# Performance work log

Measured on AMD Instinct MI355X. Metric: run time of the kernel, lower is better.

## Reference

```python
import jax, jax.numpy as jnp
import numpy as np

EPS = 1e-5
NUM_HEADS = 12

def layer_norm(x, g, b):
    mu = jnp.mean(x, axis=-1, keepdims=True)
    var = jnp.var(x, axis=-1, keepdims=True)
    return (x - mu) * jax.lax.rsqrt(var + EPS) * g + b

def setup_inputs() -> dict:
    key = jax.random.key(0)
    ks = jax.random.split(key, 8)
    B, N, Dv, Ds, F = 8, 1024, 768, 512, 768
    def w(k, shape, fan_in):
        return jax.random.normal(k, shape, jnp.float32) * (fan_in ** -0.5)
    return dict(
        visual_features=jax.random.normal(ks[0], (B, N, Dv), jnp.float32),
        semantic_features=jax.random.normal(ks[1], (B, Ds), jnp.float32),
        Wq=w(ks[2], (F, Ds), Ds),
        Wk=w(ks[3], (F, Dv), Dv),
        Wv=w(ks[4], (F, Dv), Dv),
        Wo=w(ks[5], (Dv, F), F),
        bo=jnp.zeros((Dv,), jnp.float32),
        Wg=w(ks[6], (Dv, Dv + Ds), Dv + Ds),
        bg=jnp.zeros((Dv,), jnp.float32),
        gv=jnp.ones((Dv,), jnp.float32),
        bv=jnp.zeros((Dv,), jnp.float32),
        gs=jnp.ones((Ds,), jnp.float32),
        bs=jnp.zeros((Ds,), jnp.float32),
    )

def reference(visual_features, semantic_features, Wq, Wk, Wv, Wo, bo, Wg, bg, gv, bv, gs, bs):
    B, N, Dv = visual_features.shape
    F = Wq.shape[0]
    H = NUM_HEADS
    dh = F // H
    scale = dh ** -0.5
    vis_n = layer_norm(visual_features, gv, bv)           # (B,N,Dv)
    sem_n = layer_norm(semantic_features, gs, bs)         # (B,Ds) — LN over last dim; broadcast-invariant
    # Query is identical for every patch row -> exact single-query collapse of the N x N attention
    q = (sem_n @ Wq.T).reshape(B, H, dh)                  # (B,H,dh)
    k = (vis_n @ Wk.T).reshape(B, N, H, dh).transpose(0, 2, 1, 3)  # (B,H,N,dh)
    v = (vis_n @ Wv.T).reshape(B, N, H, dh).transpose(0, 2, 1, 3)  # (B,H,N,dh)
    scores = jnp.einsum('bhd,bhnd->bhn', q, k) * scale
    attn = jax.nn.softmax(scores, axis=-1)
    ctx = jnp.einsum('bhn,bhnd->bhd', attn, v).reshape(B, F)
    attended = ctx @ Wo.T + bo                            # (B,Dv), same for all N rows (dropout in eval = identity)
    sem_b = jnp.broadcast_to(semantic_features[:, None, :], (B, N, semantic_features.shape[-1]))
    gate_in = jnp.concatenate([visual_features, sem_b], axis=-1)   # (B,N,Dv+Ds)
    gate = jax.nn.sigmoid(gate_in @ Wg.T + bg)            # (B,N,Dv)
    return visual_features + gate * attended[:, None, :]
```

## Files before the change

### kernel.cpp

```cpp
#include <hip/hip_runtime.h>
#include <hip/hip_bf16.h>
#include <math.h>


typedef __attribute__((ext_vector_type(8))) short bf16x8;
typedef __attribute__((ext_vector_type(4))) float f32x4;

#define LN_EPS 1e-5f

__device__ __forceinline__ float bf2f(__hip_bfloat16 h){ return __bfloat162float(h); }

union bfpk8 { uint4 u; __hip_bfloat16 h[8]; };
union bfpk4 { uint2 u; __hip_bfloat16 h[4]; };

__device__ __align__(16) __hip_bfloat16 c_x[8*1024*768];
__device__ __align__(16) __hip_bfloat16 c_sem[8*512];
__device__ __align__(16) __hip_bfloat16 c_Wq[768*512];
__device__ __align__(16) __hip_bfloat16 c_Wk[768*768];
__device__ __align__(16) __hip_bfloat16 c_Wv[768*768];
__device__ __align__(16) __hip_bfloat16 c_Wo[768*768];
__device__ __align__(16) __hip_bfloat16 c_bo[768];
__device__ __align__(16) __hip_bfloat16 c_Wg[768*1280];
__device__ __align__(16) __hip_bfloat16 c_bg[768];
__device__ __align__(16) __hip_bfloat16 c_gv[768];
__device__ __align__(16) __hip_bfloat16 c_bv[768];
__device__ __align__(16) __hip_bfloat16 c_gs[512];
__device__ __align__(16) __hip_bfloat16 c_bs[512];

__device__ __align__(16) __hip_bfloat16 g_gqb[8*16*768];
__device__ __align__(16) float g_A[8*12*768];
__device__ __align__(16) float g_sgq[96];
__device__ __align__(16) float g_bq[96];
__device__ __align__(16) float g_mu[8192];
__device__ __align__(16) float g_rstd[8192];
__device__ __align__(16) float g_w[8*12*1024];
__device__ __align__(16) float g_C[96];
__device__ __align__(16) float g_ctx[8*768];
__device__ __align__(16) float g_att[8*768];
__device__ __align__(16) float g_gsem[8*768];

__device__ __forceinline__ int detect_bf16(const void* gv_raw){
    return ((const unsigned int*)gv_raw)[0] == 0x3F803F80u;
}

__device__ __forceinline__ void conv8(const void* __restrict__ src,
                                      __hip_bfloat16* __restrict__ dst,
                                      int g, int isb){
    if(isb){
        ((uint4*)dst)[g] = ((const uint4*)src)[g];
    } else {
        const float* s = (const float*)src + (size_t)g*8;
        bfpk8 o;
        #pragma unroll
        for(int e=0;e<8;e++) o.h[e] = __float2bfloat16(s[e]);
        ((uint4*)dst)[g] = o.u;
    }
}

#define ING_BLKS 1925
__global__ void k_ingest(const void* s1, const void* s2, const void* s3,
                         const void* s4, const void* s5, const void* s6, const void* s7,
                         const void* s8, const void* s9, const void* s10, const void* s11,
                         const void* s12){
    int i = blockIdx.x*256 + threadIdx.x;
    int isb = detect_bf16(s9);
    if     (i <    512) conv8(s1, c_sem, i,         isb);
    else if(i <  49664) conv8(s2, c_Wq,  i-   512,  isb);
    else if(i < 123392) conv8(s3, c_Wk,  i- 49664,  isb);
    else if(i < 197120) conv8(s4, c_Wv,  i-123392,  isb);
    else if(i < 270848) conv8(s5, c_Wo,  i-197120,  isb);
    else if(i < 270944) conv8(s6, c_bo,  i-270848,  isb);
    else if(i < 393824) conv8(s7, c_Wg,  i-270944,  isb);
    else if(i < 393920) conv8(s8, c_bg,  i-393824,  isb);
    else if(i < 394016) conv8(s9, c_gv,  i-393920,  isb);
    else if(i < 394112) conv8(s10,c_bv,  i-394016,  isb);
    else if(i < 394176) conv8(s11,c_gs,  i-394112,  isb);
    else if(i < 394240) conv8(s12,c_bs,  i-394176,  isb);
    else if(i < 467968) g_A[i-394240]   = 0.f;
    else if(i < 468064) g_sgq[i-467968] = 0.f;
    else if(i < 468160) g_bq[i-468064]  = 0.f;
    else if(i < 474304) g_ctx[i-468160] = 0.f;
    else if(i < 480448) g_att[i-474304] = 0.f;
    else if(i < 492736){
        uint4 z; z.x=0; z.y=0; z.z=0; z.w=0;
        ((uint4*)g_gqb)[i-480448] = z;
    }
}

__global__ void k_qhead(){
    __shared__ float s_semn[8*512];
    __shared__ float s_q2[8][64];
    __shared__ float s_sgq[8], s_bq[8];
    const int t = threadIdx.x, h = blockIdx.y;
    {
        int b = t>>5, l = t&31;
        bfpk8 p0, p1;
        p0.u = *(const uint4*)(c_sem + b*512 + l*16);
        p1.u = *(const uint4*)(c_sem + b*512 + l*16 + 8);
        float v[16], s = 0.f, s2 = 0.f;
        #pragma unroll
        for(int e=0;e<8;e++){ v[e]   = bf2f(p0.h[e]); s += v[e];   s2 += v[e]*v[e]; }
        #pragma unroll
        for(int e=0;e<8;e++){ v[8+e] = bf2f(p1.h[e]); s += v[8+e]; s2 += v[8+e]*v[8+e]; }
        #pragma unroll
        for(int o=16;o>0;o>>=1){ s += __shfl_xor(s,o); s2 += __shfl_xor(s2,o); }
        float mu = s*(1.f/512.f);
        float rstd = rsqrtf(s2*(1.f/512.f) - mu*mu + LN_EPS);
        bfpk8 g0, g1, b0, b1;
        g0.u = *(const uint4*)(c_gs + l*16);   g1.u = *(const uint4*)(c_gs + l*16 + 8);
        b0.u = *(const uint4*)(c_bs + l*16);   b1.u = *(const uint4*)(c_bs + l*16 + 8);
        #pragma unroll
        for(int e=0;e<8;e++){
            s_semn[b*512 + l*16 + e]     = (v[e]-mu)*rstd*bf2f(g0.h[e]) + bf2f(b0.h[e]);
            s_semn[b*512 + l*16 + 8 + e] = (v[8+e]-mu)*rstd*bf2f(g1.h[e]) + bf2f(b1.h[e]);
        }
    }
    if(t < 8){ s_sgq[t] = 0.f; s_bq[t] = 0.f; }
    __syncthreads();
    {
        int fi = t & 63, bp = t >> 6;
        int f = h*64 + fi;
        const __hip_bfloat16* wr = c_Wq + (size_t)f*512;
        float a0 = 0.f, a1 = 0.f;
        for(int i0=0;i0<512;i0+=8){
            bfpk8 pk; pk.u = *(const uint4*)(wr + i0);
            #pragma unroll
            for(int c=0;c<8;c++){
                float wv = bf2f(pk.h[c]);
                a0 += wv*s_semn[bp*512 + i0 + c];
                a1 += wv*s_semn[(bp+4)*512 + i0 + c];
            }
        }
        s_q2[bp][fi] = a0; s_q2[bp+4][fi] = a1;
    }
    __syncthreads();
    int dv = blockIdx.x*256 + t;
    float acc[8] = {0,0,0,0,0,0,0,0};
    for(int j=0;j<64;j++){
        float wk = bf2f(c_Wk[(size_t)(h*64+j)*768 + dv]);
        #pragma unroll
        for(int b=0;b<8;b++) acc[b] += s_q2[b][j]*wk;
    }
    float gvv = bf2f(c_gv[dv]), bvv = bf2f(c_bv[dv]);
    #pragma unroll
    for(int b=0;b<8;b++){
        float g = acc[b]*gvv;
        g_gqb[((size_t)b*16+h)*768 + dv] = __float2bfloat16(g);
        float sg = g, sb = bvv*acc[b];
        #pragma unroll
        for(int o=32;o>0;o>>=1){ sg += __shfl_xor(sg,o); sb += __shfl_xor(sb,o); }
        if((t&63)==0){ atomicAdd(&s_sgq[b], sg); atomicAdd(&s_bq[b], sb); }
    }
    __syncthreads();
    if(t < 8){ atomicAdd(&g_sgq[t*12+h], s_sgq[t]); atomicAdd(&g_bq[t*12+h], s_bq[t]); }
}

__global__ __launch_bounds__(256)
void k_gsem(){
    __shared__ float s_sem[8*512];
    __shared__ __hip_bfloat16 s_wg[16*520];
    __shared__ float s_part[128];
    const int t = threadIdx.x;
    const int col0 = blockIdx.x*16;
    for(int i=t;i<512;i+=256){
        bfpk8 p; p.u = *(const uint4*)(c_sem + i*8);
        #pragma unroll
        for(int e=0;e<8;e++) s_sem[i*8+e] = bf2f(p.h[e]);
    }
    for(int i=t;i<16*64;i+=256){
        int rl = i>>6, c = i&63;
        *(uint4*)(s_wg + rl*520 + c*8) =
            *(const uint4*)(c_Wg + (size_t)(col0+rl)*1280 + 768 + c*8);
    }
    __syncthreads();
    const int cl = t&15, bh = t>>4, bb = bh&7, half = bh>>3;
    const __hip_bfloat16* wr = s_wg + cl*520 + half*256;
    const float* sr = s_sem + bb*512 + half*256;
    float a = 0.f;
    for(int k=0;k<256;k+=8){
        bfpk8 p; p.u = *(const uint4*)(wr + k);
        #pragma unroll
        for(int e=0;e<8;e++) a += bf2f(p.h[e])*sr[k+e];
    }
    if(half) s_part[t&127] = a;
    __syncthreads();
    if(!half) g_gsem[bb*768 + col0 + cl] = a + s_part[t&127];
}

__global__ __launch_bounds__(256)
void k_scores(const void* __restrict__ xraw, const void* __restrict__ gvraw){
    __shared__ float s_acc[256*4];
    __shared__ float s_s[4][16], s_s2[4][16];
    __shared__ float s_mu[16], s_rstd[16];
    const int b = blockIdx.y;
    const int t = threadIdx.x, lane = t & 63, w = t >> 6;
    const int isb = detect_bf16(gvraw);
    const int fr = lane & 15, quad = lane >> 4;
    const int n_tile = blockIdx.x*16;
    const size_t row = (size_t)b*1024 + n_tile + fr;
    const __hip_bfloat16* Bp = g_gqb + (size_t)b*16*768 + (size_t)fr*768;
    const int k0 = w*192;

    f32x4 acc = {};
    float s = 0.f, s2 = 0.f;
    if(isb){
        const __hip_bfloat16* xr = (const __hip_bfloat16*)xraw + row*768;
        for(int kb=k0; kb<k0+192; kb+=32){
            bfpk8 pk; pk.u = *(const uint4*)(xr + kb + quad*8);
            *(uint4*)(c_x + row*768 + kb + quad*8) = pk.u;
            #pragma unroll
            for(int e=0;e<8;e++){ float f = bf2f(pk.h[e]); s += f; s2 += f*f; }
            bf16x8 bfrag = *(const bf16x8*)(Bp + kb + quad*8);
            acc = __builtin_amdgcn_mfma_f32_16x16x32_bf16(*(const bf16x8*)&pk, bfrag, acc, 0,0,0);
        }
    } else {
        const float* xr = (const float*)xraw + row*768;
        for(int kb=k0; kb<k0+192; kb+=32){
            f32x4 x0 = *(const f32x4*)(xr + kb + quad*8);
            f32x4 x1 = *(const f32x4*)(xr + kb + quad*8 + 4);
            bfpk8 pk;
            #pragma unroll
            for(int e=0;e<4;e++){ pk.h[e]   = __float2bfloat16(x0[e]); s += x0[e]; s2 += x0[e]*x0[e]; }
            #pragma unroll
            for(int e=0;e<4;e++){ pk.h[4+e] = __float2bfloat16(x1[e]); s += x1[e]; s2 += x1[e]*x1[e]; }
            *(uint4*)(c_x + row*768 + kb + quad*8) = pk.u;
            bf16x8 bfrag = *(const bf16x8*)(Bp + kb + quad*8);
            acc = __builtin_amdgcn_mfma_f32_16x16x32_bf16(*(const bf16x8*)&pk, bfrag, acc, 0,0,0);
        }
    }
    s  += __shfl_xor(s, 16);  s  += __shfl_xor(s, 32);
    s2 += __shfl_xor(s2, 16); s2 += __shfl_xor(s2, 32);
    *(f32x4*)&s_acc[t*4] = acc;
    if(quad == 0){ s_s[w][fr] = s; s_s2[w][fr] = s2; }
    __syncthreads();
    if(w == 0){
        #pragma unroll
        for(int ww=1;ww<4;ww++){
            f32x4 o = *(const f32x4*)&s_acc[(ww*64+lane)*4];
            acc[0]+=o[0]; acc[1]+=o[1]; acc[2]+=o[2]; acc[3]+=o[3];
        }
        if(quad == 0){
            float st  = s_s[0][fr]+s_s[1][fr]+s_s[2][fr]+s_s[3][fr];
            float st2 = s_s2[0][fr]+s_s2[1][fr]+s_s2[2][fr]+s_s2[3][fr];
            float mu = st*(1.f/768.f);
            float rstd = rsqrtf(st2*(1.f/768.f) - mu*mu + LN_EPS);
            g_mu[b*1024 + n_tile + fr] = mu;
            g_rstd[b*1024 + n_tile + fr] = rstd;
            s_mu[fr] = mu; s_rstd[fr] = rstd;
        }
    }
    __syncthreads();
    if(w == 0 && fr < 12){
        float sgqh = g_sgq[b*12+fr];
        float bqh  = g_bq [b*12+fr];
        #pragma unroll
        for(int r=0;r<4;r++){
            int rr = quad*4 + r;
            float val = 0.125f*( s_rstd[rr]*(acc[r] - s_mu[rr]*sgqh) + bqh );
            g_w[((size_t)b*12+fr)*1024 + n_tile + rr] = val;
        }
    }
}

__global__ void k_softmax(){
    int bh = blockIdx.x, b = bh/12, t = threadIdx.x;
    float* sc = g_w + (size_t)bh*1024;
    f32x4 v = *(f32x4*)(sc + t*4);
    float m = fmaxf(fmaxf(v[0],v[1]), fmaxf(v[2],v[3]));
    __shared__ float redm[4], reds[4], redc[4];
    #pragma unroll
    for(int o=32;o>0;o>>=1) m = fmaxf(m, __shfl_xor(m,o));
    if((t&63)==0) redm[t>>6] = m;
    __syncthreads();
    m = fmaxf(fmaxf(redm[0],redm[1]), fmaxf(redm[2],redm[3]));
    float e0=expf(v[0]-m), e1=expf(v[1]-m), e2=expf(v[2]-m), e3=expf(v[3]-m);
    float s = e0+e1+e2+e3;
    #pragma unroll
    for(int o=32;o>0;o>>=1) s += __shfl_xor(s,o);
    if((t&63)==0) reds[t>>6] = s;
    __syncthreads();
    s = reds[0]+reds[1]+reds[2]+reds[3];
    float inv = 1.f/s;
    f32x4 rv = *(f32x4*)(g_rstd + b*1024 + t*4);
    f32x4 mv = *(f32x4*)(g_mu   + b*1024 + t*4);
    f32x4 o4;
    o4[0]=e0*inv*rv[0]; o4[1]=e1*inv*rv[1]; o4[2]=e2*inv*rv[2]; o4[3]=e3*inv*rv[3];
    *(f32x4*)(sc + t*4) = o4;
    float cp = o4[0]*mv[0] + o4[1]*mv[1] + o4[2]*mv[2] + o4[3]*mv[3];
    #pragma unroll
    for(int o=32;o>0;o>>=1) cp += __shfl_xor(cp,o);
    if((t&63)==0) redc[t>>6] = cp;
    __syncthreads();
    if(t==0) g_C[bh] = redc[0]+redc[1]+redc[2]+redc[3];
}

__global__ void k_accA(){
    __shared__ float s_w[12*128];
    int t = threadIdx.x, b = blockIdx.z, n0 = blockIdx.y*128;
    for(int i=t;i<12*128;i+=256){
        int h = i>>7, n = i&127;
        s_w[i] = g_w[((size_t)b*12+h)*1024 + n0 + n];
    }
    __syncthreads();
    int dv = blockIdx.x*256 + t;
    float acc[12] = {0,0,0,0,0,0,0,0,0,0,0,0};
    for(int n=0;n<128;n++){
        float xv = bf2f(c_x[(size_t)(b*1024+n0+n)*768 + dv]);
        #pragma unroll
        for(int h=0;h<12;h++) acc[h] += s_w[h*128+n]*xv;
    }
    #pragma unroll
    for(int h=0;h<12;h++) atomicAdd(&g_A[((size_t)b*12+h)*768 + dv], acc[h]);
}

__global__ void k_ctx(){
    __shared__ float s_wvis[8*68];
    int h = blockIdx.x, ch = blockIdx.y, t = threadIdx.x;
    int base = ch*64;
    {
        int b = t>>6, dvl = t&63;
        int dv = base + dvl;
        s_wvis[b*68+dvl] = bf2f(c_gv[dv])*(g_A[((size_t)b*12+h)*768+dv] - g_C[b*12+h]) + bf2f(c_bv[dv]);
    }
    __syncthreads();
    int f = h*64 + (t>>3), b = t&7;
    const __hip_bfloat16* wr = c_Wv + (size_t)f*768 + base;
    float acc = 0.f;
    #pragma unroll
    for(int d0=0;d0<64;d0+=8){
        bfpk8 pk; pk.u = *(const uint4*)(wr + d0);
        #pragma unroll
        for(int c=0;c<8;c++) acc += s_wvis[b*68 + d0 + c]*bf2f(pk.h[c]);
    }
    atomicAdd(&g_ctx[b*768+f], acc);
}

__global__ void k_att(){
    __shared__ float s_ctx[8*68];
    int ch = blockIdx.y, t = threadIdx.x;
    int base = ch*64;
    {
        int b = t>>6, fl = t&63;
        s_ctx[b*68+fl] = g_ctx[b*768 + base + fl];
    }
    __syncthreads();
    int dv2 = blockIdx.x*64 + (t>>3), b = t&7;
    const __hip_bfloat16* wr = c_Wo + (size_t)dv2*768 + base;
    float acc = (ch==0) ? bf2f(c_bo[dv2]) : 0.f;
    #pragma unroll
    for(int f0=0;f0<64;f0+=8){
        bfpk8 pk; pk.u = *(const uint4*)(wr + f0);
        #pragma unroll
        for(int c=0;c<8;c++) acc += s_ctx[b*68 + f0 + c]*bf2f(pk.h[c]);
    }
    atomicAdd(&g_att[b*768+dv2], acc);
}

__device__ __forceinline__ void stage_gate(int buf, int kb, int m0, int n0,
                                           __hip_bfloat16* As, __hip_bfloat16* Bs,
                                           int wave, int lane){
    const int rl = lane >> 2;
    const int kc = ((lane & 3) ^ ((rl >> 1) & 3))*8;
    #pragma unroll
    for(int s=0;s<2;s++){
        int c = wave + 4*s;
        int row = c*16 + rl;
        const __hip_bfloat16* gp = c_x + (size_t)(m0+row)*768 + kb + kc;
        __builtin_amdgcn_global_load_lds(
            (const __attribute__((address_space(1))) void*)gp,
            (__attribute__((address_space(3))) void*)(As + buf*4096 + c*512),
            16, 0, 0);
    }
    {
        int c = wave;
        int row = c*16 + rl;
        const __hip_bfloat16* gp = c_Wg + (size_t)(n0+row)*1280 + kb + kc;
        __builtin_amdgcn_global_load_lds(
            (const __attribute__((address_space(1))) void*)gp,
            (__attribute__((address_space(3))) void*)(Bs + buf*2048 + c*512),
            16, 0, 0);
    }
}

__global__ __launch_bounds__(256)
void k_gate(void* __restrict__ outv, const void* __restrict__ gv_raw){
    __shared__ __align__(16) __hip_bfloat16 As[4*128*32];
    __shared__ __align__(16) __hip_bfloat16 Bs[4*64*32];
    const int isb = detect_bf16(gv_raw);
    const int t = threadIdx.x;
    const int lin  = blockIdx.y*12 + blockIdx.x;
    const int wgid = (lin & 7)*96 + (lin >> 3);
    const int n0 = (wgid % 12)*64;
    const int m0 = (wgid / 12)*128;
    const int b_blk = m0 >> 10;
    const int lane = t & 63, wave = t >> 6;
    const int wm = (wave>>1)*64, wn = (wave&1)*32;
    const int fr = lane & 15, quad = lane >> 4;
    const int sq = (quad ^ ((fr >> 1) & 3))*8;

    f32x4 acc[4][2] = {};

    stage_gate(0,  0, m0, n0, As, Bs, wave, lane);
    stage_gate(1, 32, m0, n0, As, Bs, wave, lane);
    stage_gate(2, 64, m0, n0, As, Bs, wave, lane);
    for(int it=0; it<24; ++it){
        if(it < 22)       asm volatile("s_waitcnt vmcnt(6)" ::: "memory");
        else if(it == 22) asm volatile("s_waitcnt vmcnt(3)" ::: "memory");
        else              asm volatile("s_waitcnt vmcnt(0)" ::: "memory");
        asm volatile("s_waitcnt lgkmcnt(0)" ::: "memory");
        asm volatile("s_barrier" ::: "memory");
        const __hip_bfloat16* Ab = As + (it&3)*4096;
        const __hip_bfloat16* Bb = Bs + (it&3)*2048;
        bf16x8 af[4], bfr[2];
        #pragma unroll
        for(int i=0;i<4;i++) af[i]  = *(const bf16x8*)(Ab + (wm + i*16 + fr)*32 + sq);
        #pragma unroll
        for(int j=0;j<2;j++) bfr[j] = *(const bf16x8*)(Bb + (wn + j*16 + fr)*32 + sq);
        #pragma unroll
        for(int i=0;i<4;i++)
            #pragma unroll
            for(int j=0;j<2;j++)
                acc[i][j] = __builtin_amdgcn_mfma_f32_16x16x32_bf16(af[i], bfr[j], acc[i][j], 0,0,0);
        if(it < 21)
            stage_gate((it+3)&3, (it+3)*32, m0, n0, As, Bs, wave, lane);
    }

    #pragma unroll
    for(int j=0;j<2;j++){
        int col = n0 + wn + j*16 + fr;
        float attv = g_att[b_blk*768 + col];
        float bgv  = bf2f(c_bg[col]) + g_gsem[b_blk*768 + col];
        #pragma unroll
        for(int i=0;i<4;i++){
            int mbase = m0 + wm + i*16 + quad*4;
            #pragma unroll
            for(int r=0;r<4;r++){
                int m = mbase + r;
                float g = acc[i][j][r] + bgv;
                g = fminf(fmaxf(g, -60.f), 60.f);
                float gate = 1.f/(1.f + expf(-g));
                float xv = bf2f(c_x[(size_t)m*768 + col]);
                float val = xv + gate*attv;
                size_t idx = (size_t)m*768 + col;
                if(isb) ((__hip_bfloat16*)outv)[idx] = __float2bfloat16(val);
                else    ((float*)outv)[idx] = val;
            }
        }
    }
}

extern "C" void kernel_launch(void* const* d_in, const int* in_sizes, int n_in,
                              void* d_out, int out_size, void* d_ws, size_t ws_size,
                              hipStream_t stream){
    (void)in_sizes; (void)n_in; (void)out_size; (void)d_ws; (void)ws_size;

    k_ingest<<<dim3(ING_BLKS), dim3(256), 0, stream>>>(d_in[1], d_in[2], d_in[3],
                                                       d_in[4], d_in[5], d_in[6], d_in[7],
                                                       d_in[8], d_in[9], d_in[10], d_in[11],
                                                       d_in[12]);
    k_qhead<<<dim3(3,12), dim3(256), 0, stream>>>();
    k_gsem<<<dim3(48), dim3(256), 0, stream>>>();
    k_scores<<<dim3(64,8), dim3(256), 0, stream>>>(d_in[0], d_in[9]);
    k_softmax<<<dim3(96), dim3(256), 0, stream>>>();
    k_accA<<<dim3(3,8,8), dim3(256), 0, stream>>>();
    k_ctx<<<dim3(12,12), dim3(512), 0, stream>>>();
    k_att<<<dim3(12,12), dim3(512), 0, stream>>>();
    k_gate<<<dim3(12,64), dim3(256), 0, stream>>>(d_out, d_in[9]);
}
```

Before: 205.0 us.

## Retile q-head projection, drop split-K atomics in ctx/att, prioritize gate MFMAs

k_qhead now runs on a 12x12 grid. Each block stages a 64x64 tile of Wk in LDS and computes two batches per thread instead of eight. The old shared-memory atomic reduction becomes direct global atomics. k_ctx and k_att drop the 12-way split-K with atomicAdd: one block per head (or per output chunk) runs the full 768-long reduction and writes its result directly, which means only 12 blocks with longer serial loops. The gate GEMM wraps its MFMA block in s_setprio to favour the math waves over the loads.

```diff
diff --git a/kernel.cpp b/kernel.cpp
--- a/kernel.cpp
+++ b/kernel.cpp
@@ -87,11 +87,13 @@
     }
 }
 
-__global__ void k_qhead(){
+__global__ __launch_bounds__(256)
+void k_qhead(){
     __shared__ float s_semn[8*512];
     __shared__ float s_q2[8][64];
-    __shared__ float s_sgq[8], s_bq[8];
+    __shared__ __hip_bfloat16 s_wk[64][64];
     const int t = threadIdx.x, h = blockIdx.y;
+    const int c0 = blockIdx.x*64;
     {
         int b = t>>5, l = t&31;
         bfpk8 p0, p1;
@@ -115,7 +117,10 @@
             s_semn[b*512 + l*16 + 8 + e] = (v[8+e]-mu)*rstd*bf2f(g1.h[e]) + bf2f(b1.h[e]);
         }
     }
-    if(t < 8){ s_sgq[t] = 0.f; s_bq[t] = 0.f; }
+    for(int i=t;i<512;i+=256){
+        int j = i>>3, sl = i&7;
+        *(uint4*)(&s_wk[j][sl*8]) = *(const uint4*)(c_Wk + (size_t)(h*64+j)*768 + c0 + sl*8);
+    }
     __syncthreads();
     {
         int fi = t & 63, bp = t >> 6;
@@ -134,25 +139,32 @@
         s_q2[bp][fi] = a0; s_q2[bp+4][fi] = a1;
     }
     __syncthreads();
-    int dv = blockIdx.x*256 + t;
-    float acc[8] = {0,0,0,0,0,0,0,0};
+    const int dvl = t & 63, w = t >> 6;
+    const int dv = c0 + dvl;
+    float a0 = 0.f, a1 = 0.f;
+    #pragma unroll 8
     for(int j=0;j<64;j++){
-        float wk = bf2f(c_Wk[(size_t)(h*64+j)*768 + dv]);
-        #pragma unroll
-        for(int b=0;b<8;b++) acc[b] += s_q2[b][j]*wk;
+        float wk = bf2f(s_wk[j][dvl]);
+        a0 += s_q2[w][j]*wk;
+        a1 += s_q2[w+4][j]*wk;
     }
     float gvv = bf2f(c_gv[dv]), bvv = bf2f(c_bv[dv]);
-    #pragma unroll
-    for(int b=0;b<8;b++){
-        float g = acc[b]*gvv;
-        g_gqb[((size_t)b*16+h)*768 + dv] = __float2bfloat16(g);
-        float sg = g, sb = bvv*acc[b];
+    {
+        float g = a0*gvv;
+        g_gqb[((size_t)w*16+h)*768 + dv] = __float2bfloat16(g);
+        float sg = g, sb = bvv*a0;
         #pragma unroll
         for(int o=32;o>0;o>>=1){ sg += __shfl_xor(sg,o); sb += __shfl_xor(sb,o); }
-        if((t&63)==0){ atomicAdd(&s_sgq[b], sg); atomicAdd(&s_bq[b], sb); }
-    }
-    __syncthreads();
-    if(t < 8){ atomicAdd(&g_sgq[t*12+h], s_sgq[t]); atomicAdd(&g_bq[t*12+h], s_bq[t]); }
+        if(dvl==0){ atomicAdd(&g_sgq[w*12+h], sg); atomicAdd(&g_bq[w*12+h], sb); }
+    }
+    {
+        float g = a1*gvv;
+        g_gqb[((size_t)(w+4)*16+h)*768 + dv] = __float2bfloat16(g);
+        float sg = g, sb = bvv*a1;
+        #pragma unroll
+        for(int o=32;o>0;o>>=1){ sg += __shfl_xor(sg,o); sb += __shfl_xor(sb,o); }
+        if(dvl==0){ atomicAdd(&g_sgq[(w+4)*12+h], sg); atomicAdd(&g_bq[(w+4)*12+h], sb); }
+    }
 }
 
 __global__ __launch_bounds__(256)
@@ -314,46 +326,41 @@
 }
 
 __global__ void k_ctx(){
-    __shared__ float s_wvis[8*68];
-    int h = blockIdx.x, ch = blockIdx.y, t = threadIdx.x;
-    int base = ch*64;
-    {
-        int b = t>>6, dvl = t&63;
-        int dv = base + dvl;
-        s_wvis[b*68+dvl] = bf2f(c_gv[dv])*(g_A[((size_t)b*12+h)*768+dv] - g_C[b*12+h]) + bf2f(c_bv[dv]);
-    }
-    __syncthreads();
-    int f = h*64 + (t>>3), b = t&7;
-    const __hip_bfloat16* wr = c_Wv + (size_t)f*768 + base;
+    __shared__ float s_wvis[8][769];
+    const int h = blockIdx.x, t = threadIdx.x;
+    for(int b=0;b<8;b++){
+        float Cb = g_C[b*12+h];
+        for(int i=t;i<768;i+=512)
+            s_wvis[b][i] = bf2f(c_gv[i])*(g_A[((size_t)b*12+h)*768+i] - Cb) + bf2f(c_bv[i]);
+    }
+    __syncthreads();
+    const int f = h*64 + (t>>3), b = t&7;
+    const __hip_bfloat16* wr = c_Wv + (size_t)f*768;
     float acc = 0.f;
-    #pragma unroll
-    for(int d0=0;d0<64;d0+=8){
+    for(int d0=0;d0<768;d0+=8){
         bfpk8 pk; pk.u = *(const uint4*)(wr + d0);
         #pragma unroll
-        for(int c=0;c<8;c++) acc += s_wvis[b*68 + d0 + c]*bf2f(pk.h[c]);
-    }
-    atomicAdd(&g_ctx[b*768+f], acc);
+        for(int c=0;c<8;c++) acc += s_wvis[b][d0 + c]*bf2f(pk.h[c]);
+    }
+    g_ctx[b*768+f] = acc;
 }
 
 __global__ void k_att(){
-    __shared__ float s_ctx[8*68];
-    int ch = blockIdx.y, t = threadIdx.x;
-    int base = ch*64;
-    {
-        int b = t>>6, fl = t&63;
-        s_ctx[b*68+fl] = g_ctx[b*768 + base + fl];
-    }
-    __syncthreads();
-    int dv2 = blockIdx.x*64 + (t>>3), b = t&7;
-    const __hip_bfloat16* wr = c_Wo + (size_t)dv2*768 + base;
-    float acc = (ch==0) ? bf2f(c_bo[dv2]) : 0.f;
-    #pragma unroll
-    for(int f0=0;f0<64;f0+=8){
+    __shared__ float s_ctx[8][769];
+    const int t = threadIdx.x;
+    for(int b=0;b<8;b++)
+        for(int i=t;i<768;i+=512)
+            s_ctx[b][i] = g_ctx[b*768 + i];
+    __syncthreads();
+    const int dv2 = blockIdx.x*64 + (t>>3), b = t&7;
+    const __hip_bfloat16* wr = c_Wo + (size_t)dv2*768;
+    float acc = bf2f(c_bo[dv2]);
+    for(int f0=0;f0<768;f0+=8){
         bfpk8 pk; pk.u = *(const uint4*)(wr + f0);
         #pragma unroll
-        for(int c=0;c<8;c++) acc += s_ctx[b*68 + f0 + c]*bf2f(pk.h[c]);
-    }
-    atomicAdd(&g_att[b*768+dv2], acc);
+        for(int c=0;c<8;c++) acc += s_ctx[b][f0 + c]*bf2f(pk.h[c]);
+    }
+    g_att[b*768+dv2] = acc;
 }
 
 __device__ __forceinline__ void stage_gate(int buf, int kb, int m0, int n0,
@@ -416,11 +423,13 @@
         for(int i=0;i<4;i++) af[i]  = *(const bf16x8*)(Ab + (wm + i*16 + fr)*32 + sq);
         #pragma unroll
         for(int j=0;j<2;j++) bfr[j] = *(const bf16x8*)(Bb + (wn + j*16 + fr)*32 + sq);
+        __builtin_amdgcn_s_setprio(1);
         #pragma unroll
         for(int i=0;i<4;i++)
             #pragma unroll
             for(int j=0;j<2;j++)
                 acc[i][j] = __builtin_amdgcn_mfma_f32_16x16x32_bf16(af[i], bfr[j], acc[i][j], 0,0,0);
+        __builtin_amdgcn_s_setprio(0);
         if(it < 21)
             stage_gate((it+3)&3, (it+3)*32, m0, n0, As, Bs, wave, lane);
     }
@@ -458,12 +467,12 @@
                                                        d_in[4], d_in[5], d_in[6], d_in[7],
                                                        d_in[8], d_in[9], d_in[10], d_in[11],
                                                        d_in[12]);
-    k_qhead<<<dim3(3,12), dim3(256), 0, stream>>>();
+    k_qhead<<<dim3(12,12), dim3(256), 0, stream>>>();
     k_gsem<<<dim3(48), dim3(256), 0, stream>>>();
     k_scores<<<dim3(64,8), dim3(256), 0, stream>>>(d_in[0], d_in[9]);
     k_softmax<<<dim3(96), dim3(256), 0, stream>>>();
     k_accA<<<dim3(3,8,8), dim3(256), 0, stream>>>();
-    k_ctx<<<dim3(12,12), dim3(512), 0, stream>>>();
-    k_att<<<dim3(12,12), dim3(512), 0, stream>>>();
+    k_ctx<<<dim3(12), dim3(512), 0, stream>>>();
+    k_att<<<dim3(12), dim3(512), 0, stream>>>();
     k_gate<<<dim3(12,64), dim3(256), 0, stream>>>(d_out, d_in[9]);
 }
```

Result: slower. 228.6 us (+11.5%).

## Split k_qhead over more column blocks and stage Wk tile in LDS

Applied to the files above, without the earlier changes.

The k_qhead grid grows from 36 to 144 blocks. Each block now covers 64 output columns, with four waves each handling two batches instead of one thread handling all eight batches. The Wk slice is staged into shared memory with vectorized loads, and the shared-memory atomic reduction is replaced by direct per-wave global atomics. The aim is more parallelism in a small latency-bound kernel, at the cost of recomputing the semantic layernorm and the q projection in every block, which is four times more redundant work.

```diff
diff --git a/kernel.cpp b/kernel.cpp
--- a/kernel.cpp
+++ b/kernel.cpp
@@ -87,11 +87,13 @@
     }
 }
 
-__global__ void k_qhead(){
+__global__ __launch_bounds__(256)
+void k_qhead(){
     __shared__ float s_semn[8*512];
     __shared__ float s_q2[8][64];
-    __shared__ float s_sgq[8], s_bq[8];
+    __shared__ __hip_bfloat16 s_wk[64][64];
     const int t = threadIdx.x, h = blockIdx.y;
+    const int c0 = blockIdx.x*64;
     {
         int b = t>>5, l = t&31;
         bfpk8 p0, p1;
@@ -115,7 +117,10 @@
             s_semn[b*512 + l*16 + 8 + e] = (v[8+e]-mu)*rstd*bf2f(g1.h[e]) + bf2f(b1.h[e]);
         }
     }
-    if(t < 8){ s_sgq[t] = 0.f; s_bq[t] = 0.f; }
+    for(int i=t;i<512;i+=256){
+        int j = i>>3, sl = i&7;
+        *(uint4*)(&s_wk[j][sl*8]) = *(const uint4*)(c_Wk + (size_t)(h*64+j)*768 + c0 + sl*8);
+    }
     __syncthreads();
     {
         int fi = t & 63, bp = t >> 6;
@@ -134,25 +139,32 @@
         s_q2[bp][fi] = a0; s_q2[bp+4][fi] = a1;
     }
     __syncthreads();
-    int dv = blockIdx.x*256 + t;
-    float acc[8] = {0,0,0,0,0,0,0,0};
+    const int dvl = t & 63, w = t >> 6;
+    const int dv = c0 + dvl;
+    float a0 = 0.f, a1 = 0.f;
+    #pragma unroll 8
     for(int j=0;j<64;j++){
-        float wk = bf2f(c_Wk[(size_t)(h*64+j)*768 + dv]);
-        #pragma unroll
-        for(int b=0;b<8;b++) acc[b] += s_q2[b][j]*wk;
+        float wk = bf2f(s_wk[j][dvl]);
+        a0 += s_q2[w][j]*wk;
+        a1 += s_q2[w+4][j]*wk;
     }
     float gvv = bf2f(c_gv[dv]), bvv = bf2f(c_bv[dv]);
-    #pragma unroll
-    for(int b=0;b<8;b++){
-        float g = acc[b]*gvv;
-        g_gqb[((size_t)b*16+h)*768 + dv] = __float2bfloat16(g);
-        float sg = g, sb = bvv*acc[b];
+    {
+        float g = a0*gvv;
+        g_gqb[((size_t)w*16+h)*768 + dv] = __float2bfloat16(g);
+        float sg = g, sb = bvv*a0;
         #pragma unroll
         for(int o=32;o>0;o>>=1){ sg += __shfl_xor(sg,o); sb += __shfl_xor(sb,o); }
-        if((t&63)==0){ atomicAdd(&s_sgq[b], sg); atomicAdd(&s_bq[b], sb); }
-    }
-    __syncthreads();
-    if(t < 8){ atomicAdd(&g_sgq[t*12+h], s_sgq[t]); atomicAdd(&g_bq[t*12+h], s_bq[t]); }
+        if(dvl==0){ atomicAdd(&g_sgq[w*12+h], sg); atomicAdd(&g_bq[w*12+h], sb); }
+    }
+    {
+        float g = a1*gvv;
+        g_gqb[((size_t)(w+4)*16+h)*768 + dv] = __float2bfloat16(g);
+        float sg = g, sb = bvv*a1;
+        #pragma unroll
+        for(int o=32;o>0;o>>=1){ sg += __shfl_xor(sg,o); sb += __shfl_xor(sb,o); }
+        if(dvl==0){ atomicAdd(&g_sgq[(w+4)*12+h], sg); atomicAdd(&g_bq[(w+4)*12+h], sb); }
+    }
 }
 
 __global__ __launch_bounds__(256)
@@ -458,7 +470,7 @@
                                                        d_in[4], d_in[5], d_in[6], d_in[7],
                                                        d_in[8], d_in[9], d_in[10], d_in[11],
                                                        d_in[12]);
-    k_qhead<<<dim3(3,12), dim3(256), 0, stream>>>();
+    k_qhead<<<dim3(12,12), dim3(256), 0, stream>>>();
     k_gsem<<<dim3(48), dim3(256), 0, stream>>>();
     k_scores<<<dim3(64,8), dim3(256), 0, stream>>>(d_in[0], d_in[9]);
     k_softmax<<<dim3(96), dim3(256), 0, stream>>>();
```

After: 201.9 us. Within noise of the previous version (-1.5%).
